# Kernel tuning notes

Hardware: AMD Instinct MI355X
Metric: run time of the kernel (lower is better)

Reference implementation:

```python
import jax, jax.numpy as jnp
import numpy as np

B, T, X, H, Z = 64, 2048, 128, 256, 64


def setup_inputs() -> dict:
    key = jax.random.key(0)
    ks = jax.random.split(key, 6)
    s = lambda n: 1.0 / np.sqrt(n).astype(np.float32)
    return {
        "x_seq": jax.random.normal(ks[0], (B, T, X), jnp.float32),
        # LSTMCell params packed as [i|f|g|o] gates. Flax: input dense has no bias,
        # hidden dense has bias.
        "Wi": jax.random.normal(ks[1], (X, 4 * H), jnp.float32) * s(X),
        "Wh": jax.random.normal(ks[2], (H, 4 * H), jnp.float32) * s(H),
        "bh": jnp.zeros((4 * H,), jnp.float32),
        # head: Dense(H) -> relu -> Dense(2Z)
        "W1": jax.random.normal(ks[3], (H, H), jnp.float32) * s(H),
        "b1": jnp.zeros((H,), jnp.float32),
        "W2": jax.random.normal(ks[4], (H, 2 * Z), jnp.float32) * s(H),
        "b2": jnp.zeros((2 * Z,), jnp.float32),
    }


def _forward(x_seq, Wi, Wh, bh, W1, b1, W2, b2):
    Bsz = x_seq.shape[0]
    Hd = Wh.shape[0]
    # Precompute input projection for all timesteps (one big GEMM).
    x_proj = jnp.einsum('btx,xg->btg', x_seq, Wi)  # (B, T, 4H)
    xp = jnp.swapaxes(x_proj, 0, 1)  # (T, B, 4H) for scan

    def step(carry, xp_t):
        c, h = carry
        gates = xp_t + h @ Wh + bh  # (B, 4H)
        i, f, g, o = jnp.split(gates, 4, axis=-1)
        i = jax.nn.sigmoid(i)
        f = jax.nn.sigmoid(f)
        g = jnp.tanh(g)
        o = jax.nn.sigmoid(o)
        c = f * c + i * g
        h = o * jnp.tanh(c)
        hid = jax.nn.relu(h @ W1 + b1)
        out = hid @ W2 + b2  # (B, 2Z)
        return (c, h), out

    c0 = jnp.zeros((Bsz, Hd), x_seq.dtype)
    h0 = jnp.zeros((Bsz, Hd), x_seq.dtype)
    _, outs = jax.lax.scan(step, (c0, h0), xp)  # outs: (T, B, 2Z)
    outs = jnp.swapaxes(outs, 0, 1)  # (B, T, 2Z)
    mu_seq, log_sigma_seq = jnp.split(outs, 2, axis=-1)
    return mu_seq, log_sigma_seq


def reference(x_seq, Wi, Wh, bh, W1, b1, W2, b2):
    return _forward(x_seq, Wi, Wh, bh, W1, b1, W2, b2)
```

## Files before the change

### kernel.cpp

```cpp
#include <hip/hip_runtime.h>

typedef _Float16 f16;
typedef _Float16 h2 __attribute__((ext_vector_type(2)));
typedef _Float16 h8 __attribute__((ext_vector_type(8)));
typedef float f4 __attribute__((ext_vector_type(4)));

constexpr int Bb = 64, Tt = 2048, Xx = 128, Hh = 256, G4 = 1024, Z2 = 128;

__device__ __forceinline__ float fdot2f(h2 a, h2 b, float c) {
#if __has_builtin(__builtin_amdgcn_fdot2)
  return __builtin_amdgcn_fdot2(a, b, c, false);
#else
  return c + (float)a[0] * (float)b[0] + (float)a[1] * (float)b[1];
#endif
}
__device__ __forceinline__ float tanhf_(float x) {
  float e = __expf(2.0f * x);
  return 1.0f - 2.0f * __builtin_amdgcn_rcpf(e + 1.0f);
}
__device__ __forceinline__ h2 bch2(unsigned int u) { return __builtin_bit_cast(h2, u); }

template <int CTRL>
__device__ __forceinline__ float qb(float v) {
  return __builtin_bit_cast(float,
      __builtin_amdgcn_mov_dpp(__builtin_bit_cast(int, v), CTRL, 0xf, 0xf, true));
}

__global__ void cast_f16_k(const float* __restrict__ in, f16* __restrict__ out, int n) {
  int i = (blockIdx.x * 256 + threadIdx.x) * 4;
  if (i >= n) return;
  float4 v = *(const float4*)(in + i);
  h2 a = {(f16)v.x, (f16)v.y};
  h2 b = {(f16)v.z, (f16)v.w};
  uint2 o = {__builtin_bit_cast(unsigned int, a), __builtin_bit_cast(unsigned int, b)};
  *(uint2*)(out + i) = o;
}

__global__ void cast_wiP_k(const float* __restrict__ Wi, f16* __restrict__ out) {
  int idx = blockIdx.x * 256 + threadIdx.x;
  int k = idx >> 10, cp = idx & 1023;
  out[idx] = (f16)Wi[(long)k * G4 + (cp & 3) * 256 + (cp >> 2)];
}
__global__ void cast_bhp_k(const float* __restrict__ bh, float* __restrict__ bhp) {
  int cp = blockIdx.x * 256 + threadIdx.x;
  bhp[cp] = bh[(cp & 3) * 256 + (cp >> 2)];
}

__global__ void cast_whT2_k(const float* __restrict__ Wh, f16* __restrict__ WhT2) {
  int idx = blockIdx.x * 256 + threadIdx.x;
  int tid = idx >> 9, f = idx & 511;
  int s = f >> 1, e = f & 1;
  int c_off, k;
  if (s < 96)      { c_off = 0; k = 2 * s + e; }
  else if (s < 192){ c_off = 1; k = 2 * (s - 96) + e; }
  else if (s < 224){ c_off = 0; k = 192 + 2 * (s - 192) + e; }
  else             { c_off = 1; k = 192 + 2 * (s - 224) + e; }
  int cc = 2 * tid + c_off;
  int j = cc >> 2, g = cc & 3;
  WhT2[(long)tid * 512 + f] = (f16)Wh[(long)k * G4 + g * 256 + j];
}

__global__ void cast_whQ_k(const float* __restrict__ Wh, f16* __restrict__ Wq) {
  int idx = blockIdx.x * 256 + threadIdx.x;
  int st = idx >> 8, k = idx & 255;
  int tid = st & 511, hb = st >> 9;
  int j = hb * 128 + (tid >> 2), g = tid & 3;
  Wq[(long)st * 256 + k] = (f16)Wh[(long)k * G4 + g * 256 + j];
}

__global__ __launch_bounds__(256, 4) void gemm_f16_k(
    const f16* __restrict__ A, const f16* __restrict__ Bm, const float* __restrict__ bias,
    f16* __restrict__ C16, float* __restrict__ Cmu, float* __restrict__ Cls,
    int N, int K, int a_shift, int a_ostride, int a_t0,
    int mode, int o_t0, int tcshift)
{
  __shared__ __align__(16) f16 At[64][48];
  __shared__ __align__(16) f16 Bt[64][48];
  const int tid = threadIdx.x;
  const int mblk = blockIdx.x, nblk = blockIdx.y;
  const int w = tid >> 6, lane = tid & 63;

  const int sa_row = tid >> 2, sa_k = (tid & 3) * 8;
  const int m_g = mblk * 64 + sa_row;
  const long arow = (long)(m_g >> a_shift) * a_ostride + a_t0 + (m_g & ((1 << a_shift) - 1));
  const f16* aptr = A + arow * K + sa_k;
  const int sb_k = tid >> 3, sb_n = (tid & 7) * 8;
  const f16* bptr = Bm + (long)sb_k * N + nblk * 64 + sb_n;

  f4 acc[4];
#pragma unroll
  for (int i = 0; i < 4; ++i) acc[i] = (f4){0.f, 0.f, 0.f, 0.f};

  const int arow_l = w * 16 + (lane & 15);
  const int k0 = (lane >> 4) * 8;

  for (int kk = 0; kk < K; kk += 32) {
    uint4 av = *(const uint4*)(aptr + kk);
    uint4 bv = *(const uint4*)(bptr + (long)kk * N);
    __syncthreads();
    *(uint4*)&At[sa_row][sa_k] = av;
    h8 bx = __builtin_bit_cast(h8, bv);
#pragma unroll
    for (int j = 0; j < 8; ++j) Bt[sb_n + j][sb_k] = bx[j];
    __syncthreads();
    h8 af = *(const h8*)&At[arow_l][k0];
#pragma unroll
    for (int nt = 0; nt < 4; ++nt) {
      h8 bf = *(const h8*)&Bt[nt * 16 + (lane & 15)][k0];
      acc[nt] = __builtin_amdgcn_mfma_f32_16x16x32_f16(af, bf, acc[nt], 0, 0, 0);
    }
  }

  const int row_l = w * 16 + ((lane >> 4) << 2);
  const int col_l = lane & 15;
#pragma unroll
  for (int nt = 0; nt < 4; ++nt) {
    int gcol = nblk * 64 + nt * 16 + col_l;
    float bv = bias[gcol];
#pragma unroll
    for (int r = 0; r < 4; ++r) {
      int gm = mblk * 64 + row_l + r;
      float val = acc[nt][r] + bv;
      if (mode == 1) val = fmaxf(val, 0.f);
      if (mode <= 1) {
        C16[(long)gm * N + gcol] = (f16)val;
      } else {
        int bb = gm >> tcshift, tl = gm & ((1 << tcshift) - 1);
        long orow = (long)bb * Tt + o_t0 + tl;
        if (gcol < 64) Cmu[orow * 64 + gcol] = val;
        else Cls[orow * 64 + (gcol - 64)] = val;
      }
    }
  }
}

__global__ void __launch_bounds__(512, 2) lstm_split_k(
    const f16* __restrict__ Wq, const f16* __restrict__ xp,
    f16* __restrict__ hout, float* __restrict__ c_state, f16* __restrict__ h_state,
    unsigned int* __restrict__ pub, int TC, int first)
{
  const int bid = blockIdx.x;
  const int b = bid & 63, hb = bid >> 6;
  const int tid = threadIdx.x;
  const int u = tid >> 2, g = tid & 3;
  const int gu = hb * 128 + u;
  __shared__ __align__(16) h2 hbuf[2][128];
  __shared__ uint4 wt[10][512];

  h2 w[96];
  {
    const uint4* p4 = (const uint4*)(Wq + (long)(hb * 512 + tid) * 256);
#pragma unroll
    for (int i = 0; i < 24; ++i) {
      uint4 v = p4[i];
      w[4 * i + 0] = bch2(v.x); w[4 * i + 1] = bch2(v.y);
      w[4 * i + 2] = bch2(v.z); w[4 * i + 3] = bch2(v.w);
    }
#pragma unroll
    for (int r = 0; r < 8; ++r) wt[r][tid] = p4[24 + r];
  }

  float c = first ? 0.f : c_state[b * Hh + gu];
  if (tid < 128) {
    h2 hz = {(f16)0.f, (f16)0.f};
    hbuf[0][tid] = first ? hz : ((const h2*)h_state)[b * 128 + tid];
  }
  __syncthreads();

  const float sgn = (g == 2) ? 2.0f : -1.0f;
  const int xcol = hb * 512 + tid;
  const f16* xptr = xp + (long)b * TC * G4 + xcol;
  const f16* xend = xptr + (long)(TC - 1) * G4;
  f16 xc = *xptr;
  unsigned int* pub_own = pub + ((b * 2 + hb) * 2) * 128;
  unsigned int* pub_par = pub + ((b * 2 + (hb ^ 1)) * 2) * 128;
  int p = 0;
  for (int t = 0; t < TC; ++t) {
    const f16* xnp = (xptr == xend) ? xptr : xptr + G4;
    f16 xn = *xnp;

    float a0 = (float)xc, b0 = 0.f;
    const uint4* hb4 = (const uint4*)&hbuf[p][0];
#pragma unroll
    for (int i = 0; i < 24; ++i) {
      uint4 hv = hb4[i];
      a0 = fdot2f(w[4 * i + 0], bch2(hv.x), a0);
      b0 = fdot2f(w[4 * i + 1], bch2(hv.y), b0);
      a0 = fdot2f(w[4 * i + 2], bch2(hv.z), a0);
      b0 = fdot2f(w[4 * i + 3], bch2(hv.w), b0);
    }
#pragma unroll
    for (int r = 0; r < 8; ++r) {
      uint4 hv = hb4[24 + r];
      uint4 wv = wt[r][tid];
      a0 = fdot2f(bch2(wv.x), bch2(hv.x), a0);
      b0 = fdot2f(bch2(wv.y), bch2(hv.y), b0);
      a0 = fdot2f(bch2(wv.z), bch2(hv.z), a0);
      b0 = fdot2f(bch2(wv.w), bch2(hv.w), b0);
    }
    float A = a0 + b0;

    float e = __expf(sgn * A);
    float r0 = __builtin_amdgcn_rcpf(1.0f + e);
    float act = (g == 2) ? 1.0f - 2.0f * r0 : r0;

    float ai = qb<0x00>(act), af = qb<0x55>(act);
    float ag = qb<0xAA>(act), ao = qb<0xFF>(act);
    c = af * c + ai * ag;
    float hval = ao * tanhf_(c);

    f16 hh = (f16)hval;
    if (g == 0) {
      ((f16*)&hbuf[p ^ 1][0])[gu] = hh;
      unsigned word = ((unsigned)(t + 1) << 16) |
                      (unsigned)__builtin_bit_cast(unsigned short, hh);
      __hip_atomic_store(&pub_own[(t & 1) * 128 + u], word,
                         __ATOMIC_RELAXED, __HIP_MEMORY_SCOPE_AGENT);
      hout[((long)b * TC + t) * Hh + gu] = hh;
    }
    if (tid < 128) {
      const unsigned want = (unsigned)(t + 1);
      unsigned v;
      while (((v = __hip_atomic_load(&pub_par[(t & 1) * 128 + tid],
                                     __ATOMIC_RELAXED,
                                     __HIP_MEMORY_SCOPE_AGENT)) >> 16) != want)
        __builtin_amdgcn_s_sleep(2);
      ((f16*)&hbuf[p ^ 1][0])[(hb ^ 1) * 128 + tid] =
          __builtin_bit_cast(f16, (unsigned short)(v & 0xffffu));
    }
    __syncthreads();
    p ^= 1;
    xc = xn;
    xptr = xnp;
  }
  if (g == 0) c_state[b * Hh + gu] = c;
  if (tid < 128 && hb == 0)
    ((h2*)h_state)[b * 128 + tid] = hbuf[p][tid];
}

__global__ void __launch_bounds__(512, 2) lstm512_k(
    const f16* __restrict__ WhT2, const f16* __restrict__ xp,
    f16* __restrict__ hout, float* __restrict__ c_state, f16* __restrict__ h_state,
    int TC, int first)
{
  const int b = blockIdx.x, tid = threadIdx.x;
  const int j = tid >> 1, odd = tid & 1;
  __shared__ __align__(16) h2 hbuf[2][128];
  __shared__ uint4 wt[16][512];

  h2 w[192];
  {
    const uint4* p4 = (const uint4*)(WhT2 + (long)tid * 512);
#pragma unroll
    for (int u = 0; u < 48; ++u) {
      uint4 v = p4[u];
      w[4 * u + 0] = bch2(v.x); w[4 * u + 1] = bch2(v.y);
      w[4 * u + 2] = bch2(v.z); w[4 * u + 3] = bch2(v.w);
    }
#pragma unroll
    for (int gg = 0; gg < 16; ++gg) wt[gg][tid] = p4[48 + gg];
  }

  float c = first ? 0.f : c_state[b * Hh + j];
  if (tid < 128) {
    h2 hz = {(f16)0.f, (f16)0.f};
    hbuf[0][tid] = first ? hz : ((const h2*)h_state)[b * 128 + tid];
  }
  __syncthreads();

  const float sgn0 = odd ? 2.0f : -1.0f;
  const f16* xptr = xp + (long)b * TC * G4 + 2 * tid;
  const f16* xend = xptr + (long)(TC - 1) * G4;
  h2 xv = *(const h2*)xptr;
  int p = 0;
  for (int t = 0; t < TC; ++t) {
    const f16* xnp = (xptr == xend) ? xptr : xptr + G4;
    h2 xn = *(const h2*)xnp;

    float a0 = (float)xv[0], b0 = 0.f, a1 = (float)xv[1], b1 = 0.f;
    const uint4* hb4 = (const uint4*)&hbuf[p][0];
#pragma unroll
    for (int i = 0; i < 24; ++i) {
      uint4 hv = hb4[i];
      a0 = fdot2f(w[4 * i + 0], bch2(hv.x), a0);
      b0 = fdot2f(w[4 * i + 1], bch2(hv.y), b0);
      a0 = fdot2f(w[4 * i + 2], bch2(hv.z), a0);
      b0 = fdot2f(w[4 * i + 3], bch2(hv.w), b0);
      a1 = fdot2f(w[96 + 4 * i + 0], bch2(hv.x), a1);
      b1 = fdot2f(w[96 + 4 * i + 1], bch2(hv.y), b1);
      a1 = fdot2f(w[96 + 4 * i + 2], bch2(hv.z), a1);
      b1 = fdot2f(w[96 + 4 * i + 3], bch2(hv.w), b1);
    }
#pragma unroll
    for (int gg = 0; gg < 8; ++gg) {
      uint4 hv = hb4[24 + gg];
      uint4 wa = wt[gg][tid];
      uint4 wb = wt[8 + gg][tid];
      a0 = fdot2f(bch2(wa.x), bch2(hv.x), a0);
      b0 = fdot2f(bch2(wa.y), bch2(hv.y), b0);
      a0 = fdot2f(bch2(wa.z), bch2(hv.z), a0);
      b0 = fdot2f(bch2(wa.w), bch2(hv.w), b0);
      a1 = fdot2f(bch2(wb.x), bch2(hv.x), a1);
      b1 = fdot2f(bch2(wb.y), bch2(hv.y), b1);
      a1 = fdot2f(bch2(wb.z), bch2(hv.z), a1);
      b1 = fdot2f(bch2(wb.w), bch2(hv.w), b1);
    }
    float A0 = a0 + b0, A1 = a1 + b1;

    float e0 = __expf(sgn0 * A0);
    float r0 = __builtin_amdgcn_rcpf(1.0f + e0);
    float act0 = odd ? 1.0f - 2.0f * r0 : r0;
    float e1 = __expf(-A1);
    float act1 = __builtin_amdgcn_rcpf(1.0f + e1);

    float px0 = qb<0xB1>(act0), px1 = qb<0xB1>(act1);
    float ai = odd ? px0 : act0;
    float af = odd ? px1 : act1;
    float ag = odd ? act0 : px0;
    float ao = odd ? act1 : px1;
    c = af * c + ai * ag;
    float hval = ao * tanhf_(c);
    if (!odd) {
      f16 hh = (f16)hval;
      ((f16*)&hbuf[p ^ 1][0])[j] = hh;
      hout[((long)b * TC + t) * Hh + j] = hh;
    }
    __syncthreads();
    p ^= 1;
    xv = xn;
    xptr = xnp;
  }
  if (!odd) c_state[b * Hh + j] = c;
  if (tid < 128) ((h2*)h_state)[b * 128 + tid] = hbuf[p][tid];
}

extern "C" void kernel_launch(void* const* d_in, const int* in_sizes, int n_in,
                              void* d_out, int out_size, void* d_ws, size_t ws_size,
                              hipStream_t stream)
{
  const float* x  = (const float*)d_in[0];
  const float* Wi = (const float*)d_in[1];
  const float* Wh = (const float*)d_in[2];
  const float* bh = (const float*)d_in[3];
  const float* W1 = (const float*)d_in[4];
  const float* b1 = (const float*)d_in[5];
  const float* W2 = (const float*)d_in[6];
  const float* b2 = (const float*)d_in[7];
  float* out = (float*)d_out;

  char* ws = (char*)d_ws;
  size_t off = 0;
  auto alloc = [&](size_t bytes) -> char* {
    char* p = ws + off;
    off = (off + bytes + 255) & ~(size_t)255;
    return p;
  };
  f16* x16    = (f16*)alloc((size_t)Bb * Tt * Xx * 2);
  f16* wi16p  = (f16*)alloc((size_t)Xx * G4 * 2);
  float* bhp  = (float*)alloc((size_t)G4 * 4);
  f16* whT2   = (f16*)alloc((size_t)G4 * Hh * 2);
  f16* whQ    = (f16*)alloc((size_t)G4 * Hh * 2);
  f16* w116   = (f16*)alloc((size_t)Hh * Hh * 2);
  f16* w216   = (f16*)alloc((size_t)Hh * Z2 * 2);
  float* cst  = (float*)alloc((size_t)Bb * Hh * 4);
  f16* hst    = (f16*)alloc((size_t)Bb * Hh * 2);
  const size_t PUBSZ = (size_t)Bb * 2 * 2 * 128 * 4;
  unsigned int* pub = (unsigned int*)alloc(PUBSZ);

  int tc = 1024;
  while (tc > 32) {
    size_t need = (size_t)Bb * tc * G4 * 2 + (size_t)Bb * tc * Hh * 2;
    if (off + need <= ws_size) break;
    tc >>= 1;
  }
  int tcsh = __builtin_ctz((unsigned)tc);
  f16* xp16 = (f16*)alloc((size_t)Bb * tc * G4 * 2);
  f16* h16  = (f16*)alloc((size_t)Bb * tc * Hh * 2);
  f16* hid16 = xp16;

  cast_f16_k<<<(Bb * Tt * Xx) / 1024, 256, 0, stream>>>(x, x16, Bb * Tt * Xx);
  cast_wiP_k<<<(Xx * G4) / 256, 256, 0, stream>>>(Wi, wi16p);
  cast_bhp_k<<<4, 256, 0, stream>>>(bh, bhp);
  cast_f16_k<<<(Hh * Hh) / 1024, 256, 0, stream>>>(W1, w116, Hh * Hh);
  cast_f16_k<<<(Hh * Z2) / 1024, 256, 0, stream>>>(W2, w216, Hh * Z2);
  cast_whT2_k<<<(Hh * G4) / 256, 256, 0, stream>>>(Wh, whT2);
  cast_whQ_k<<<(Hh * G4) / 256, 256, 0, stream>>>(Wh, whQ);

  float* mu = out;
  float* ls = out + (size_t)Bb * Tt * 64;

  int ci = 0;
  for (int t0 = 0; t0 < Tt; t0 += tc, ++ci) {
    dim3 gx(Bb * tc / 64, G4 / 64);
    gemm_f16_k<<<gx, 256, 0, stream>>>(x16, wi16p, bhp, xp16, nullptr, nullptr,
                                       G4, Xx, tcsh, Tt, t0, 0, 0, 0);
    if (ci == 0) {
      hipMemsetAsync(pub, 0, PUBSZ, stream);
      lstm_split_k<<<128, 512, 0, stream>>>(whQ, xp16, h16, cst, hst, pub, tc,
                                            (t0 == 0) ? 1 : 0);
    } else {
      lstm512_k<<<Bb, 512, 0, stream>>>(whT2, xp16, h16, cst, hst, tc,
                                        (t0 == 0) ? 1 : 0);
    }
    dim3 g1g(Bb * tc / 64, Hh / 64);
    gemm_f16_k<<<g1g, 256, 0, stream>>>(h16, w116, b1, hid16, nullptr, nullptr,
                                        Hh, Hh, 30, 0, 0, 1, 0, 0);
    dim3 g2g(Bb * tc / 64, Z2 / 64);
    gemm_f16_k<<<g2g, 256, 0, stream>>>(hid16, w216, b2, nullptr, mu, ls,
                                        Z2, Hh, 30, 0, 0, 2, t0, tcsh);
  }
}
```

Measured before the change: 3.132 ms.

## Overlap partner hidden-state wait with local-half dot products in split LSTM

Reorders the per-block recurrent weights so each block first accumulates the dot product over its own half of h, which it already holds in LDS. Only then does it spin on the partner block's published values and finish with the partner half. The partner's h for step t is now consumed at the start of step t+1 rather than at the end of step t. This hides cross-block handoff latency behind useful compute, at the cost of an extra __syncthreads per timestep.

```diff
diff --git a/kernel.cpp b/kernel.cpp
--- a/kernel.cpp
+++ b/kernel.cpp
@@ -60,12 +60,13 @@
   WhT2[(long)tid * 512 + f] = (f16)Wh[(long)k * G4 + g * 256 + j];
 }
 
-__global__ void cast_whQ_k(const float* __restrict__ Wh, f16* __restrict__ Wq) {
+__global__ void cast_whR_k(const float* __restrict__ Wh, f16* __restrict__ Wq) {
   int idx = blockIdx.x * 256 + threadIdx.x;
-  int st = idx >> 8, k = idx & 255;
+  int st = idx >> 8, pos = idx & 255;
   int tid = st & 511, hb = st >> 9;
   int j = hb * 128 + (tid >> 2), g = tid & 3;
-  Wq[(long)st * 256 + k] = (f16)Wh[(long)k * G4 + g * 256 + j];
+  int k = (128 * hb + pos) & 255;
+  Wq[(long)st * 256 + pos] = (f16)Wh[(long)k * G4 + g * 256 + j];
 }
 
 __global__ __launch_bounds__(256, 4) void gemm_f16_k(
@@ -134,7 +135,7 @@
   }
 }
 
-__global__ void __launch_bounds__(512, 2) lstm_split_k(
+__global__ void __launch_bounds__(512, 2) lstm_splitp_k(
     const f16* __restrict__ Wq, const f16* __restrict__ xp,
     f16* __restrict__ hout, float* __restrict__ c_state, f16* __restrict__ h_state,
     unsigned int* __restrict__ pub, int TC, int first)
@@ -168,8 +169,7 @@
   __syncthreads();
 
   const float sgn = (g == 2) ? 2.0f : -1.0f;
-  const int xcol = hb * 512 + tid;
-  const f16* xptr = xp + (long)b * TC * G4 + xcol;
+  const f16* xptr = xp + (long)b * TC * G4 + hb * 512 + tid;
   const f16* xend = xptr + (long)(TC - 1) * G4;
   f16 xc = *xptr;
   unsigned int* pub_own = pub + ((b * 2 + hb) * 2) * 128;
@@ -179,19 +179,41 @@
     const f16* xnp = (xptr == xend) ? xptr : xptr + G4;
     f16 xn = *xnp;
 
+    const uint4* ho = (const uint4*)&hbuf[p][0] + hb * 16;
+    const uint4* hq = (const uint4*)&hbuf[p][0] + (hb ^ 1) * 16;
     float a0 = (float)xc, b0 = 0.f;
-    const uint4* hb4 = (const uint4*)&hbuf[p][0];
-#pragma unroll
-    for (int i = 0; i < 24; ++i) {
-      uint4 hv = hb4[i];
+#pragma unroll
+    for (int i = 0; i < 16; ++i) {
+      uint4 hv = ho[i];
       a0 = fdot2f(w[4 * i + 0], bch2(hv.x), a0);
       b0 = fdot2f(w[4 * i + 1], bch2(hv.y), b0);
       a0 = fdot2f(w[4 * i + 2], bch2(hv.z), a0);
       b0 = fdot2f(w[4 * i + 3], bch2(hv.w), b0);
     }
+
+    if (t > 0 && tid < 128) {
+      const unsigned want = (unsigned)t;
+      unsigned v;
+      while (((v = __hip_atomic_load(&pub_par[(t & 1) * 128 + tid],
+                                     __ATOMIC_RELAXED,
+                                     __HIP_MEMORY_SCOPE_AGENT)) >> 16) != want)
+        __builtin_amdgcn_s_sleep(1);
+      ((f16*)&hbuf[p][0])[(hb ^ 1) * 128 + tid] =
+          __builtin_bit_cast(f16, (unsigned short)(v & 0xffffu));
+    }
+    __syncthreads();
+
+#pragma unroll
+    for (int i = 0; i < 8; ++i) {
+      uint4 hv = hq[i];
+      a0 = fdot2f(w[64 + 4 * i + 0], bch2(hv.x), a0);
+      b0 = fdot2f(w[64 + 4 * i + 1], bch2(hv.y), b0);
+      a0 = fdot2f(w[64 + 4 * i + 2], bch2(hv.z), a0);
+      b0 = fdot2f(w[64 + 4 * i + 3], bch2(hv.w), b0);
+    }
 #pragma unroll
     for (int r = 0; r < 8; ++r) {
-      uint4 hv = hb4[24 + r];
+      uint4 hv = hq[8 + r];
       uint4 wv = wt[r][tid];
       a0 = fdot2f(bch2(wv.x), bch2(hv.x), a0);
       b0 = fdot2f(bch2(wv.y), bch2(hv.y), b0);
@@ -209,24 +231,14 @@
     c = af * c + ai * ag;
     float hval = ao * tanhf_(c);
 
-    f16 hh = (f16)hval;
     if (g == 0) {
+      f16 hh = (f16)hval;
       ((f16*)&hbuf[p ^ 1][0])[gu] = hh;
-      unsigned word = ((unsigned)(t + 1) << 16) |
+      unsigned word = ((unsigned)(t + 2 - 1) << 16) |
                       (unsigned)__builtin_bit_cast(unsigned short, hh);
-      __hip_atomic_store(&pub_own[(t & 1) * 128 + u], word,
+      __hip_atomic_store(&pub_own[((t + 1) & 1) * 128 + u], word,
                          __ATOMIC_RELAXED, __HIP_MEMORY_SCOPE_AGENT);
       hout[((long)b * TC + t) * Hh + gu] = hh;
-    }
-    if (tid < 128) {
-      const unsigned want = (unsigned)(t + 1);
-      unsigned v;
-      while (((v = __hip_atomic_load(&pub_par[(t & 1) * 128 + tid],
-                                     __ATOMIC_RELAXED,
-                                     __HIP_MEMORY_SCOPE_AGENT)) >> 16) != want)
-        __builtin_amdgcn_s_sleep(2);
-      ((f16*)&hbuf[p ^ 1][0])[(hb ^ 1) * 128 + tid] =
-          __builtin_bit_cast(f16, (unsigned short)(v & 0xffffu));
     }
     __syncthreads();
     p ^= 1;
@@ -234,8 +246,8 @@
     xptr = xnp;
   }
   if (g == 0) c_state[b * Hh + gu] = c;
-  if (tid < 128 && hb == 0)
-    ((h2*)h_state)[b * 128 + tid] = hbuf[p][tid];
+  if (tid < 64)
+    ((h2*)h_state)[b * 128 + hb * 64 + tid] = hbuf[p][hb * 64 + tid];
 }
 
 __global__ void __launch_bounds__(512, 2) lstm512_k(
@@ -359,7 +371,7 @@
   f16* wi16p  = (f16*)alloc((size_t)Xx * G4 * 2);
   float* bhp  = (float*)alloc((size_t)G4 * 4);
   f16* whT2   = (f16*)alloc((size_t)G4 * Hh * 2);
-  f16* whQ    = (f16*)alloc((size_t)G4 * Hh * 2);
+  f16* whR    = (f16*)alloc((size_t)G4 * Hh * 2);
   f16* w116   = (f16*)alloc((size_t)Hh * Hh * 2);
   f16* w216   = (f16*)alloc((size_t)Hh * Z2 * 2);
   float* cst  = (float*)alloc((size_t)Bb * Hh * 4);
@@ -384,7 +396,7 @@
   cast_f16_k<<<(Hh * Hh) / 1024, 256, 0, stream>>>(W1, w116, Hh * Hh);
   cast_f16_k<<<(Hh * Z2) / 1024, 256, 0, stream>>>(W2, w216, Hh * Z2);
   cast_whT2_k<<<(Hh * G4) / 256, 256, 0, stream>>>(Wh, whT2);
-  cast_whQ_k<<<(Hh * G4) / 256, 256, 0, stream>>>(Wh, whQ);
+  cast_whR_k<<<(Hh * G4) / 256, 256, 0, stream>>>(Wh, whR);
 
   float* mu = out;
   float* ls = out + (size_t)Bb * Tt * 64;
@@ -396,8 +408,8 @@
                                        G4, Xx, tcsh, Tt, t0, 0, 0, 0);
     if (ci == 0) {
       hipMemsetAsync(pub, 0, PUBSZ, stream);
-      lstm_split_k<<<128, 512, 0, stream>>>(whQ, xp16, h16, cst, hst, pub, tc,
-                                            (t0 == 0) ? 1 : 0);
+      lstm_splitp_k<<<128, 512, 0, stream>>>(whR, xp16, h16, cst, hst, pub, tc,
+                                             (t0 == 0) ? 1 : 0);
     } else {
       lstm512_k<<<Bb, 512, 0, stream>>>(whT2, xp16, h16, cst, hst, tc,
                                         (t0 == 0) ? 1 : 0);
```

Measured after the change: 3.149 ms. No clear change (+0.5%).
